# Kernel optimization log

Hardware: AMD Instinct MI355X
Metric: run time of the kernel (lower is better)

## Reference

```python
import jax, jax.numpy as jnp
import numpy as np

DIM = 768
N_IMGS = 1024
N_PATCH = 196
GRID = int(np.sqrt(N_PATCH))  # 14
B = 64


def setup_inputs() -> dict:
    key = jax.random.key(0)
    ks = jax.random.split(key, 12)
    x = jax.random.normal(ks[0], (B, N_PATCH, DIM), dtype=jnp.float32)
    mask = jnp.ones((B, N_PATCH), dtype=jnp.bool_)
    img_ids = jax.random.randint(ks[1], (B,), 0, N_IMGS, dtype=jnp.int32)
    eps = jax.random.normal(ks[2], (B, 2, N_PATCH), dtype=jnp.float32)
    s = 0.02
    Wq = jax.random.normal(ks[3], (DIM, DIM), dtype=jnp.float32) * s
    bq = jnp.zeros((DIM,), dtype=jnp.float32)
    Wk = jax.random.normal(ks[4], (DIM, DIM), dtype=jnp.float32) * s
    bk = jnp.zeros((DIM,), dtype=jnp.float32)
    Wv = jax.random.normal(ks[5], (DIM, DIM), dtype=jnp.float32) * s
    bv = jnp.zeros((DIM,), dtype=jnp.float32)
    # per-image Gaussian location params: means in [0, GRID-1], small positive stds
    avgs = jax.random.uniform(ks[6], (N_IMGS, 2, N_PATCH), dtype=jnp.float32) * (GRID - 1)
    std_devs = jax.random.uniform(ks[7], (N_IMGS, 2, N_PATCH), dtype=jnp.float32) * 1.5 + 0.1
    return {"x": x, "mask": mask, "img_ids": img_ids, "eps": eps,
            "Wq": Wq, "bq": bq, "Wk": Wk, "bk": bk, "Wv": Wv, "bv": bv,
            "avgs": avgs, "std_devs": std_devs}


def reference(x, mask, img_ids, eps, Wq, bq, Wk, bk, Wv, bv, avgs, std_devs):
    # projections: (B,S,D)
    q = jnp.einsum('bsd,ed->bse', x, Wq) + bq
    k = jnp.einsum('bsd,ed->bse', x, Wk) + bk
    v = jnp.einsum('bsd,ed->bse', x, Wv) + bv

    # sample per-query key coordinates: torch.normal(mean, std) == mean + std * eps
    mu = avgs[img_ids]        # (B,2,S)
    sd = std_devs[img_ids]    # (B,2,S)
    coord = mu + sd * eps     # (B,2,S)
    kx, ky = coord[:, 0], coord[:, 1]           # each (B,S)
    kx1, kx2 = jnp.ceil(kx), jnp.floor(kx)
    ky1, ky2 = jnp.ceil(ky), jnp.floor(ky)

    # 4 interpolation-corner flat indices per query: grid*y + x  -> (B,S,4)
    idx = jnp.stack([GRID * ky1 + kx1,
                     GRID * ky1 + kx2,
                     GRID * ky2 + kx1,
                     GRID * ky2 + kx2], axis=-1)
    idx = jnp.clip(idx, 0, N_PATCH - 1).astype(jnp.int32)

    bidx = jnp.arange(idx.shape[0])[:, None, None]  # (B,1,1)
    sampled_k = k[bidx, idx]  # (B,S,4,D)
    sampled_v = v[bidx, idx]  # (B,S,4,D)

    # softmax over the 4 sampled keys (elementwise per feature), weighted sum of values
    w = jax.nn.softmax(q[:, :, None, :] * sampled_k, axis=2)  # (B,S,4,D)
    out = jnp.sum(w * sampled_v, axis=2)                      # (B,S,D)
    return out
```

## Files before the change

kernel.cpp:

```cpp
#include <hip/hip_runtime.h>
#include <hip/hip_bf16.h>

typedef _Float16 f16;
typedef f16 f16x4 __attribute__((ext_vector_type(4)));
typedef f16 f16x8 __attribute__((ext_vector_type(8)));
typedef float f32x4 __attribute__((ext_vector_type(4)));

#define DIM   768
#define NP    196
#define BATCH 64
#define MROWS (BATCH * NP)
#define NCOLS (3 * DIM)
#define GRIDF 14.0f

#define NX4  (MROWS * DIM / 4)
#define NW4  (DIM * DIM / 4)
#define NCVT (NX4 + 3 * NW4)

__global__ __launch_bounds__(256) void convert_inputs(
    const float* __restrict__ x,
    const float* __restrict__ Wq, const float* __restrict__ Wk, const float* __restrict__ Wv,
    f16* __restrict__ x_h, f16* __restrict__ W_h) {
  int i = blockIdx.x * 256 + threadIdx.x;
  if (i >= NCVT) return;
  const float* src;
  f16* dst;
  int j;
  if (i < NX4) {
    src = x; dst = x_h; j = i;
  } else {
    j = i - NX4;
    if (j < NW4)          { src = Wq; dst = W_h; }
    else if (j < 2 * NW4) { src = Wk; dst = W_h + DIM * DIM;     j -= NW4; }
    else                  { src = Wv; dst = W_h + 2 * DIM * DIM; j -= 2 * NW4; }
  }
  float4 v = ((const float4*)src)[j];
  f16x4 h;
  h[0] = (f16)v.x; h[1] = (f16)v.y; h[2] = (f16)v.z; h[3] = (f16)v.w;
  ((f16x4*)dst)[j] = h;
}


#define BM 256
#define BN 256
#define BK 64
#define NT    (DIM / BK)
#define NITER (NT / 2)

__device__ __forceinline__ void gl_lds16(const f16* g, f16* l) {
  __builtin_amdgcn_global_load_lds(
      (const __attribute__((address_space(1))) void*)g,
      (__attribute__((address_space(3))) void*)l, 16, 0, 0);
}

#define MFMA16(acc_, av, bv) acc_ = __builtin_amdgcn_mfma_f32_16x16x32_f16(av, bv, acc_, 0, 0, 0)
#define BAR    __builtin_amdgcn_s_barrier()
#define LGKM0  asm volatile("s_waitcnt lgkmcnt(0)" ::: "memory")
#define VMCNT4 asm volatile("s_waitcnt vmcnt(4)" ::: "memory")
#define VMCNT0 asm volatile("s_waitcnt vmcnt(0)" ::: "memory")

__global__ __launch_bounds__(512, 2) void gemm_qkv(
    const f16* __restrict__ A, const f16* __restrict__ W,
    const float* __restrict__ bq, const float* __restrict__ bk, const float* __restrict__ bv,
    f16* __restrict__ C) {
  __shared__ f16 sA[2][BM * BK];
  __shared__ f16 sB[2][BN * BK];

  const int t    = threadIdx.x;
  const int lane = t & 63;
  const int wid  = t >> 6;
  const int wr   = wid >> 2;
  const int wc   = wid & 3;

  const int nwg = 49 * 9, qq = nwg / 8, rr = nwg % 8;
  const int xcd = blockIdx.x & 7, seq = blockIdx.x >> 3;
  const int logical = (xcd < rr ? xcd * (qq + 1) : rr * (qq + 1) + (xcd - rr) * qq) + seq;
  const int bm0 = (logical / 9) * BM;
  const int bn0 = (logical % 9) * BN;

  const int srow  = t >> 3;
  const int sslot = t & 7;
  const int gcol  = 8 * (sslot ^ (srow & 7));
  const int lds_off = srow * BK + sslot * 8;
  const f16* gAr = A + (size_t)(bm0 + srow) * DIM + gcol;
  const f16* gBr = W + (size_t)(bn0 + srow) * DIM + gcol;

#define STAGE_A(kt, h) do {                                          \
    const f16* _g = gAr + (size_t)((h) * 128) * DIM + (kt) * BK;     \
    f16* _l = &sA[(kt) & 1][(h) * 128 * BK + lds_off];               \
    gl_lds16(_g, _l);                                                \
    gl_lds16(_g + (size_t)64 * DIM, _l + 64 * BK);                   \
  } while (0)

#define STAGE_B(kt, h) do {                                          \
    const f16* _g = gBr + (size_t)((h) * 128) * DIM + (kt) * BK;     \
    f16* _l = &sB[(kt) & 1][(h) * 128 * BK + lds_off];               \
    gl_lds16(_g, _l);                                                \
    gl_lds16(_g + (size_t)64 * DIM, _l + 64 * BK);                   \
  } while (0)

  const int rl = lane & 15;
  const int kg = lane >> 4;
  const int s7 = lane & 7;
  const int slot0 = ((0 * 4 + kg) ^ s7) * 8;
  const int slot1 = ((1 * 4 + kg) ^ s7) * 8;
  const int aBase = (wr * 128 + rl) * BK;
  const int bBase = (wc * 64 + rl) * BK;

  f32x4 acc[8][4] = {};
  f16x8 afr[2][2], bfr[4][2];

#define LDB(buf) do {                                                            \
    _Pragma("unroll") for (int ni = 0; ni < 4; ++ni) {                           \
      bfr[ni][0] = *(const f16x8*)&sB[buf][bBase + ni * 16 * BK + slot0];        \
      bfr[ni][1] = *(const f16x8*)&sB[buf][bBase + ni * 16 * BK + slot1];        \
    } } while (0)

#define LDA(buf, q_) do {                                                        \
    _Pragma("unroll") for (int mm = 0; mm < 2; ++mm) {                           \
      afr[mm][0] = *(const f16x8*)&sA[buf][aBase + ((q_) * 2 + mm) * 16 * BK + slot0]; \
      afr[mm][1] = *(const f16x8*)&sA[buf][aBase + ((q_) * 2 + mm) * 16 * BK + slot1]; \
    } } while (0)

#define MMA(q_) do {                                                             \
    __builtin_amdgcn_s_setprio(1);                                               \
    _Pragma("unroll") for (int ni = 0; ni < 4; ++ni) {                           \
      MFMA16(acc[(q_) * 2 + 0][ni], afr[0][0], bfr[ni][0]);                      \
      MFMA16(acc[(q_) * 2 + 1][ni], afr[1][0], bfr[ni][0]);                      \
      MFMA16(acc[(q_) * 2 + 0][ni], afr[0][1], bfr[ni][1]);                      \
      MFMA16(acc[(q_) * 2 + 1][ni], afr[1][1], bfr[ni][1]);                      \
    }                                                                            \
    __builtin_amdgcn_s_setprio(0); } while (0)

  STAGE_A(0, 0); STAGE_A(0, 1); STAGE_B(0, 0); STAGE_B(0, 1);
  STAGE_B(1, 0); STAGE_B(1, 1);
  VMCNT4;
  BAR;

  for (int i = 0; i < NITER; ++i) {
    const int t1 = 2 * i + 1;
    const bool more = (i + 1 < NITER);
    LDB(0); LDA(0, 0); STAGE_A(t1, 0);
    BAR; LGKM0; MMA(0); BAR;
    LDA(0, 1); STAGE_A(t1, 1);
    BAR; LGKM0; MMA(1); BAR;
    LDA(0, 2); if (more) STAGE_B(t1 + 1, 0);
    BAR; LGKM0; MMA(2); BAR;
    LDA(0, 3); if (more) STAGE_B(t1 + 1, 1);
    BAR; LGKM0; MMA(3);
    if (more) { VMCNT4; } else { VMCNT0; }
    BAR;
    LDB(1); LDA(1, 0); if (more) STAGE_A(t1 + 1, 0);
    BAR; LGKM0; MMA(0); BAR;
    LDA(1, 1); if (more) STAGE_A(t1 + 1, 1);
    BAR; LGKM0; MMA(1); BAR;
    LDA(1, 2); if (more) STAGE_B(t1 + 2, 0);
    BAR; LGKM0; MMA(2); BAR;
    LDA(1, 3); if (more) STAGE_B(t1 + 2, 1);
    BAR; LGKM0; MMA(3); VMCNT4; BAR;
  }

#pragma unroll
  for (int ni = 0; ni < 4; ++ni) {
    const int n = bn0 + wc * 64 + ni * 16 + rl;
    const float bias = (n < DIM) ? bq[n] : ((n < 2 * DIM) ? bk[n - DIM] : bv[n - 2 * DIM]);
#pragma unroll
    for (int mi = 0; mi < 8; ++mi) {
      const int mbase = bm0 + wr * 128 + mi * 16 + 4 * kg;
#pragma unroll
      for (int v = 0; v < 4; ++v)
        C[(size_t)(mbase + v) * NCOLS + n] = (f16)(acc[mi][ni][v] + bias);
    }
  }
}

__global__ __launch_bounds__(256) void attend(
    const f16* __restrict__ qkv,
    const int* __restrict__ img_ids, const float* __restrict__ eps,
    const float* __restrict__ avgs, const float* __restrict__ stds,
    float* __restrict__ out) {
  const int lane = threadIdx.x & 63;
  const int wid  = threadIdx.x >> 6;
  const int gw = blockIdx.x * 4 + wid;
  const int b = gw / NP;
  const int s = gw - b * NP;

  const int img = img_ids[b];
  const float ex = eps[(b * 2 + 0) * NP + s];
  const float ey = eps[(b * 2 + 1) * NP + s];
  const float mux = avgs[(img * 2 + 0) * NP + s];
  const float muy = avgs[(img * 2 + 1) * NP + s];
  const float sdx = stds[(img * 2 + 0) * NP + s];
  const float sdy = stds[(img * 2 + 1) * NP + s];

  const float kx = fmaf(sdx, ex, mux);
  const float ky = fmaf(sdy, ey, muy);
  const float kx1 = ceilf(kx), kx2 = floorf(kx);
  const float ky1 = ceilf(ky), ky2 = floorf(ky);

  int idx[4];
  idx[0] = (int)fminf(fmaxf(GRIDF * ky1 + kx1, 0.0f), 195.0f);
  idx[1] = (int)fminf(fmaxf(GRIDF * ky1 + kx2, 0.0f), 195.0f);
  idx[2] = (int)fminf(fmaxf(GRIDF * ky2 + kx1, 0.0f), 195.0f);
  idx[3] = (int)fminf(fmaxf(GRIDF * ky2 + kx2, 0.0f), 195.0f);

  const f16* qrow = qkv + (size_t)gw * NCOLS;
  const f16* base = qkv + (size_t)(b * NP) * NCOLS;
  const f16* k0p = base + (size_t)idx[0] * NCOLS + DIM;
  const f16* k1p = base + (size_t)idx[1] * NCOLS + DIM;
  const f16* k2p = base + (size_t)idx[2] * NCOLS + DIM;
  const f16* k3p = base + (size_t)idx[3] * NCOLS + DIM;
  const f16* v0p = k0p + DIM;
  const f16* v1p = k1p + DIM;
  const f16* v2p = k2p + DIM;
  const f16* v3p = k3p + DIM;
  float* orow = out + (size_t)gw * DIM;

#pragma unroll
  for (int seg = 0; seg < 3; ++seg) {
    const int e0 = seg * 256 + lane * 4;
    f16x4 qv  = *(const f16x4*)(qrow + e0);
    f16x4 kv0 = *(const f16x4*)(k0p + e0);
    f16x4 kv1 = *(const f16x4*)(k1p + e0);
    f16x4 kv2 = *(const f16x4*)(k2p + e0);
    f16x4 kv3 = *(const f16x4*)(k3p + e0);
    f16x4 vv0 = *(const f16x4*)(v0p + e0);
    f16x4 vv1 = *(const f16x4*)(v1p + e0);
    f16x4 vv2 = *(const f16x4*)(v2p + e0);
    f16x4 vv3 = *(const f16x4*)(v3p + e0);
    float4 o;
    float* op = &o.x;
#pragma unroll
    for (int c = 0; c < 4; ++c) {
      const float q = (float)qv[c];
      const float s0 = q * (float)kv0[c];
      const float s1 = q * (float)kv1[c];
      const float s2 = q * (float)kv2[c];
      const float s3 = q * (float)kv3[c];
      const float mx = fmaxf(fmaxf(s0, s1), fmaxf(s2, s3));
      const float w0 = __expf(s0 - mx);
      const float w1 = __expf(s1 - mx);
      const float w2 = __expf(s2 - mx);
      const float w3 = __expf(s3 - mx);
      const float den = w0 + w1 + w2 + w3;
      const float num = w0 * (float)vv0[c] + w1 * (float)vv1[c] +
                        w2 * (float)vv2[c] + w3 * (float)vv3[c];
      op[c] = num / den;
    }
    *(float4*)(orow + e0) = o;
  }
}

extern "C" void kernel_launch(void* const* d_in, const int* in_sizes, int n_in,
                              void* d_out, int out_size, void* d_ws, size_t ws_size,
                              hipStream_t stream) {
  const float* x       = (const float*)d_in[0];
  const int*   img_ids = (const int*)d_in[2];
  const float* eps     = (const float*)d_in[3];
  const float* Wq      = (const float*)d_in[4];
  const float* bq      = (const float*)d_in[5];
  const float* Wk      = (const float*)d_in[6];
  const float* bk      = (const float*)d_in[7];
  const float* Wv      = (const float*)d_in[8];
  const float* bv      = (const float*)d_in[9];
  const float* avgs    = (const float*)d_in[10];
  const float* stds    = (const float*)d_in[11];
  float* out = (float*)d_out;

  char* ws = (char*)d_ws;
  const size_t XH_BYTES = (size_t)MROWS * DIM * 2;
  const size_t WH_BYTES = (size_t)NCOLS * DIM * 2;
  f16* x_h = (f16*)ws;
  f16* W_h = (f16*)(ws + XH_BYTES);
  f16* qkv = (f16*)(ws + XH_BYTES + WH_BYTES);

  {
    int grid = (NCVT + 255) / 256;
    convert_inputs<<<grid, 256, 0, stream>>>(x, Wq, Wk, Wv, x_h, W_h);
  }
  {
    gemm_qkv<<<441, 512, 0, stream>>>(x_h, W_h, bq, bk, bv, qkv);
  }
  {
    int grid = MROWS / 4;
    attend<<<grid, 256, 0, stream>>>(qkv, img_ids, eps, avgs, stds, out);
  }
}
```

Before: 101.8 us.

## Fuse fp32-to-fp16 conversion of x into GEMM A-tile loads and coalesce epilogue

Measured after the change: 96.21 us. 5.5% less time.

```diff
diff --git a/kernel.cpp b/kernel.cpp
--- a/kernel.cpp
+++ b/kernel.cpp
@@ -13,31 +13,34 @@
 #define NCOLS (3 * DIM)
 #define GRIDF 14.0f
 
-#define NX4  (MROWS * DIM / 4)
-#define NW4  (DIM * DIM / 4)
-#define NCVT (NX4 + 3 * NW4)
-
-__global__ __launch_bounds__(256) void convert_inputs(
-    const float* __restrict__ x,
+#define NW4   (DIM * DIM / 4)
+#define NB4   (NCOLS / 4)
+#define NWCVT (3 * NW4 + NB4)
+
+__global__ __launch_bounds__(256) void convert_w(
     const float* __restrict__ Wq, const float* __restrict__ Wk, const float* __restrict__ Wv,
-    f16* __restrict__ x_h, f16* __restrict__ W_h) {
+    const float* __restrict__ bq, const float* __restrict__ bk, const float* __restrict__ bv,
+    f16* __restrict__ W_h, float* __restrict__ bias_all) {
   int i = blockIdx.x * 256 + threadIdx.x;
-  if (i >= NCVT) return;
-  const float* src;
-  f16* dst;
-  int j;
-  if (i < NX4) {
-    src = x; dst = x_h; j = i;
-  } else {
-    j = i - NX4;
+  if (i >= NWCVT) return;
+  if (i < 3 * NW4) {
+    const float* src;
+    f16* dst;
+    int j = i;
     if (j < NW4)          { src = Wq; dst = W_h; }
     else if (j < 2 * NW4) { src = Wk; dst = W_h + DIM * DIM;     j -= NW4; }
     else                  { src = Wv; dst = W_h + 2 * DIM * DIM; j -= 2 * NW4; }
-  }
-  float4 v = ((const float4*)src)[j];
-  f16x4 h;
-  h[0] = (f16)v.x; h[1] = (f16)v.y; h[2] = (f16)v.z; h[3] = (f16)v.w;
-  ((f16x4*)dst)[j] = h;
+    float4 v = ((const float4*)src)[j];
+    f16x4 h;
+    h[0] = (f16)v.x; h[1] = (f16)v.y; h[2] = (f16)v.z; h[3] = (f16)v.w;
+    ((f16x4*)dst)[j] = h;
+  } else {
+    int j = i - 3 * NW4;
+    float4 v = (j < 192) ? ((const float4*)bq)[j]
+             : (j < 384) ? ((const float4*)bk)[j - 192]
+                         : ((const float4*)bv)[j - 384];
+    ((float4*)bias_all)[j] = v;
+  }
 }
 
 
@@ -59,12 +62,13 @@
 #define VMCNT4 asm volatile("s_waitcnt vmcnt(4)" ::: "memory")
 #define VMCNT0 asm volatile("s_waitcnt vmcnt(0)" ::: "memory")
 
+#define sAoff(buf) ((buf) * (BM * BK))
+#define sBoff(buf) (2 * BM * BK + (buf) * (BN * BK))
+
 __global__ __launch_bounds__(512, 2) void gemm_qkv(
-    const f16* __restrict__ A, const f16* __restrict__ W,
-    const float* __restrict__ bq, const float* __restrict__ bk, const float* __restrict__ bv,
-    f16* __restrict__ C) {
-  __shared__ f16 sA[2][BM * BK];
-  __shared__ f16 sB[2][BN * BK];
+    const float* __restrict__ X, const f16* __restrict__ W,
+    const float* __restrict__ bias_all, f16* __restrict__ C) {
+  __shared__ __align__(16) f16 lds[2 * BM * BK + 2 * BN * BK];
 
   const int t    = threadIdx.x;
   const int lane = t & 63;
@@ -82,21 +86,35 @@
   const int sslot = t & 7;
   const int gcol  = 8 * (sslot ^ (srow & 7));
   const int lds_off = srow * BK + sslot * 8;
-  const f16* gAr = A + (size_t)(bm0 + srow) * DIM + gcol;
   const f16* gBr = W + (size_t)(bn0 + srow) * DIM + gcol;
 
-#define STAGE_A(kt, h) do {                                          \
-    const f16* _g = gAr + (size_t)((h) * 128) * DIM + (kt) * BK;     \
-    f16* _l = &sA[(kt) & 1][(h) * 128 * BK + lds_off];               \
-    gl_lds16(_g, _l);                                                \
-    gl_lds16(_g + (size_t)64 * DIM, _l + 64 * BK);                   \
+  float4 pA0, pA1, pA2, pA3, pA4, pA5, pA6, pA7;
+
+#define A_ISSUE(kt) do {                                                      \
+    const float* _g0 = X + (size_t)(bm0 + srow) * DIM + (kt) * BK + gcol;     \
+    pA0 = *(const float4*)_g0;               pA1 = *(const float4*)(_g0 + 4); \
+    pA2 = *(const float4*)(_g0 + 64 * DIM);  pA3 = *(const float4*)(_g0 + 64 * DIM + 4);  \
+    pA4 = *(const float4*)(_g0 + 128 * DIM); pA5 = *(const float4*)(_g0 + 128 * DIM + 4); \
+    pA6 = *(const float4*)(_g0 + 192 * DIM); pA7 = *(const float4*)(_g0 + 192 * DIM + 4); \
   } while (0)
 
-#define STAGE_B(kt, h) do {                                          \
-    const f16* _g = gBr + (size_t)((h) * 128) * DIM + (kt) * BK;     \
-    f16* _l = &sB[(kt) & 1][(h) * 128 * BK + lds_off];               \
-    gl_lds16(_g, _l);                                                \
-    gl_lds16(_g + (size_t)64 * DIM, _l + 64 * BK);                   \
+#define CVT8(dst_, lo_, hi_) do {                                  \
+    dst_[0]=(f16)lo_.x; dst_[1]=(f16)lo_.y; dst_[2]=(f16)lo_.z; dst_[3]=(f16)lo_.w; \
+    dst_[4]=(f16)hi_.x; dst_[5]=(f16)hi_.y; dst_[6]=(f16)hi_.z; dst_[7]=(f16)hi_.w; } while (0)
+
+#define A_WRITE(kt, h) do {                                                   \
+    f16x8 _h0, _h1;                                                           \
+    if ((h) == 0) { CVT8(_h0, pA0, pA1); CVT8(_h1, pA2, pA3); }               \
+    else          { CVT8(_h0, pA4, pA5); CVT8(_h1, pA6, pA7); }               \
+    f16* _l = &lds[sAoff((kt) & 1) + (h) * 128 * BK + lds_off];               \
+    *(f16x8*)_l = _h0; *(f16x8*)(_l + 64 * BK) = _h1;                         \
+  } while (0)
+
+#define STAGE_B(kt, h) do {                                                   \
+    const f16* _g = gBr + (size_t)((h) * 128) * DIM + (kt) * BK;              \
+    f16* _l = &lds[sBoff((kt) & 1) + (h) * 128 * BK + lds_off];               \
+    gl_lds16(_g, _l);                                                         \
+    gl_lds16(_g + (size_t)64 * DIM, _l + 64 * BK);                            \
   } while (0)
 
   const int rl = lane & 15;
@@ -110,39 +128,44 @@
   f32x4 acc[8][4] = {};
   f16x8 afr[2][2], bfr[4][2];
 
-#define LDB(buf) do {                                                            \
-    _Pragma("unroll") for (int ni = 0; ni < 4; ++ni) {                           \
-      bfr[ni][0] = *(const f16x8*)&sB[buf][bBase + ni * 16 * BK + slot0];        \
-      bfr[ni][1] = *(const f16x8*)&sB[buf][bBase + ni * 16 * BK + slot1];        \
+#define LDB(buf) do {                                                                   \
+    _Pragma("unroll") for (int ni = 0; ni < 4; ++ni) {                                  \
+      bfr[ni][0] = *(const f16x8*)&lds[sBoff(buf) + bBase + ni * 16 * BK + slot0];      \
+      bfr[ni][1] = *(const f16x8*)&lds[sBoff(buf) + bBase + ni * 16 * BK + slot1];      \
     } } while (0)
 
-#define LDA(buf, q_) do {                                                        \
-    _Pragma("unroll") for (int mm = 0; mm < 2; ++mm) {                           \
-      afr[mm][0] = *(const f16x8*)&sA[buf][aBase + ((q_) * 2 + mm) * 16 * BK + slot0]; \
-      afr[mm][1] = *(const f16x8*)&sA[buf][aBase + ((q_) * 2 + mm) * 16 * BK + slot1]; \
+#define LDA(buf, q_) do {                                                               \
+    _Pragma("unroll") for (int mm = 0; mm < 2; ++mm) {                                  \
+      afr[mm][0] = *(const f16x8*)&lds[sAoff(buf) + aBase + ((q_) * 2 + mm) * 16 * BK + slot0]; \
+      afr[mm][1] = *(const f16x8*)&lds[sAoff(buf) + aBase + ((q_) * 2 + mm) * 16 * BK + slot1]; \
     } } while (0)
 
-#define MMA(q_) do {                                                             \
-    __builtin_amdgcn_s_setprio(1);                                               \
-    _Pragma("unroll") for (int ni = 0; ni < 4; ++ni) {                           \
-      MFMA16(acc[(q_) * 2 + 0][ni], afr[0][0], bfr[ni][0]);                      \
-      MFMA16(acc[(q_) * 2 + 1][ni], afr[1][0], bfr[ni][0]);                      \
-      MFMA16(acc[(q_) * 2 + 0][ni], afr[0][1], bfr[ni][1]);                      \
-      MFMA16(acc[(q_) * 2 + 1][ni], afr[1][1], bfr[ni][1]);                      \
-    }                                                                            \
+#define MMA(q_) do {                                                                    \
+    __builtin_amdgcn_s_setprio(1);                                                      \
+    _Pragma("unroll") for (int ni = 0; ni < 4; ++ni) {                                  \
+      MFMA16(acc[(q_) * 2 + 0][ni], bfr[ni][0], afr[0][0]);                             \
+      MFMA16(acc[(q_) * 2 + 1][ni], bfr[ni][0], afr[1][0]);                             \
+      MFMA16(acc[(q_) * 2 + 0][ni], bfr[ni][1], afr[0][1]);                             \
+      MFMA16(acc[(q_) * 2 + 1][ni], bfr[ni][1], afr[1][1]);                             \
+    }                                                                                   \
     __builtin_amdgcn_s_setprio(0); } while (0)
 
-  STAGE_A(0, 0); STAGE_A(0, 1); STAGE_B(0, 0); STAGE_B(0, 1);
+  A_ISSUE(0);
+  STAGE_B(0, 0); STAGE_B(0, 1);
   STAGE_B(1, 0); STAGE_B(1, 1);
+  A_WRITE(0, 0); A_WRITE(0, 1);
   VMCNT4;
+  LGKM0;
   BAR;
 
   for (int i = 0; i < NITER; ++i) {
     const int t1 = 2 * i + 1;
     const bool more = (i + 1 < NITER);
-    LDB(0); LDA(0, 0); STAGE_A(t1, 0);
+    A_ISSUE(t1);
+    LDB(0); LDA(0, 0);
+    A_WRITE(t1, 0);
     BAR; LGKM0; MMA(0); BAR;
-    LDA(0, 1); STAGE_A(t1, 1);
+    LDA(0, 1); A_WRITE(t1, 1);
     BAR; LGKM0; MMA(1); BAR;
     LDA(0, 2); if (more) STAGE_B(t1 + 1, 0);
     BAR; LGKM0; MMA(2); BAR;
@@ -150,9 +173,11 @@
     BAR; LGKM0; MMA(3);
     if (more) { VMCNT4; } else { VMCNT0; }
     BAR;
-    LDB(1); LDA(1, 0); if (more) STAGE_A(t1 + 1, 0);
+    if (more) A_ISSUE(t1 + 1);
+    LDB(1); LDA(1, 0);
+    if (more) A_WRITE(t1 + 1, 0);
     BAR; LGKM0; MMA(0); BAR;
-    LDA(1, 1); if (more) STAGE_A(t1 + 1, 1);
+    LDA(1, 1); if (more) A_WRITE(t1 + 1, 1);
     BAR; LGKM0; MMA(1); BAR;
     LDA(1, 2); if (more) STAGE_B(t1 + 2, 0);
     BAR; LGKM0; MMA(2); BAR;
@@ -160,16 +185,32 @@
     BAR; LGKM0; MMA(3); VMCNT4; BAR;
   }
 
-#pragma unroll
-  for (int ni = 0; ni < 4; ++ni) {
-    const int n = bn0 + wc * 64 + ni * 16 + rl;
-    const float bias = (n < DIM) ? bq[n] : ((n < 2 * DIM) ? bk[n - DIM] : bv[n - 2 * DIM]);
-#pragma unroll
-    for (int mi = 0; mi < 8; ++mi) {
-      const int mbase = bm0 + wr * 128 + mi * 16 + 4 * kg;
-#pragma unroll
-      for (int v = 0; v < 4; ++v)
-        C[(size_t)(mbase + v) * NCOLS + n] = (f16)(acc[mi][ni][v] + bias);
+  {
+    const int mloc0 = wr * 128 + rl;
+    const int nq0   = wc * 64 + 4 * kg;
+#pragma unroll
+    for (int ni = 0; ni < 4; ++ni) {
+      const int nloc = nq0 + ni * 16;
+      const float4 b4 = *(const float4*)&bias_all[bn0 + nloc];
+#pragma unroll
+      for (int mi = 0; mi < 8; ++mi) {
+        const int m = mloc0 + mi * 16;
+        f16x4 h;
+        h[0] = (f16)(acc[mi][ni][0] + b4.x);
+        h[1] = (f16)(acc[mi][ni][1] + b4.y);
+        h[2] = (f16)(acc[mi][ni][2] + b4.z);
+        h[3] = (f16)(acc[mi][ni][3] + b4.w);
+        *(f16x4*)&lds[m * 256 + (nloc ^ ((m & 7) << 3))] = h;
+      }
+    }
+    LGKM0; BAR;
+    const int rrow = t >> 5;
+    const int rchk = t & 31;
+#pragma unroll
+    for (int p = 0; p < 16; ++p) {
+      const int row = p * 16 + rrow;
+      f16x8 vdat = *(const f16x8*)&lds[row * 256 + ((rchk * 8) ^ ((row & 7) << 3))];
+      *(f16x8*)&C[(size_t)(bm0 + row) * NCOLS + bn0 + rchk * 8] = vdat;
     }
   }
 }
@@ -181,7 +222,8 @@
     float* __restrict__ out) {
   const int lane = threadIdx.x & 63;
   const int wid  = threadIdx.x >> 6;
-  const int gw = blockIdx.x * 4 + wid;
+  const int logical = (blockIdx.x & 7) * 392 + (blockIdx.x >> 3);
+  const int gw = logical * 4 + wid;
   const int b = gw / NP;
   const int s = gw - b * NP;
 
@@ -268,18 +310,18 @@
   float* out = (float*)d_out;
 
   char* ws = (char*)d_ws;
-  const size_t XH_BYTES = (size_t)MROWS * DIM * 2;
   const size_t WH_BYTES = (size_t)NCOLS * DIM * 2;
-  f16* x_h = (f16*)ws;
-  f16* W_h = (f16*)(ws + XH_BYTES);
-  f16* qkv = (f16*)(ws + XH_BYTES + WH_BYTES);
+  const size_t BI_BYTES = (size_t)NCOLS * 4;
+  f16*   W_h      = (f16*)ws;
+  float* bias_all = (float*)(ws + WH_BYTES);
+  f16*   qkv      = (f16*)(ws + WH_BYTES + BI_BYTES);
 
   {
-    int grid = (NCVT + 255) / 256;
-    convert_inputs<<<grid, 256, 0, stream>>>(x, Wq, Wk, Wv, x_h, W_h);
+    int grid = (NWCVT + 255) / 256;
+    convert_w<<<grid, 256, 0, stream>>>(Wq, Wk, Wv, bq, bk, bv, W_h, bias_all);
   }
   {
-    gemm_qkv<<<441, 512, 0, stream>>>(x_h, W_h, bq, bk, bv, qkv);
+    gemm_qkv<<<441, 512, 0, stream>>>(x, W_h, bias_all, qkv);
   }
   {
     int grid = MROWS / 4;
```
